# Kernel tuning notes

Hardware: AMD Instinct MI355X
Metric: run time of the kernel (lower is better)

Reference implementation:

```python
import jax, jax.numpy as jnp
import numpy as np

N = 100000
E = 1600000
F_IN = 64
H = 128
D_OUT = 1
G = 512  # number of graphs
EPS = 1e-5


def setup_inputs() -> dict:
    key = jax.random.key(0)
    ks = jax.random.split(key, 16)
    x = jax.random.normal(ks[0], (N, F_IN), dtype=jnp.float32)
    edge_index = jax.random.randint(ks[1], (2, E), 0, N, dtype=jnp.int64)
    batch = jnp.sort(jax.random.randint(ks[2], (N,), 0, G, dtype=jnp.int64))
    def lin(k, fin, fout):
        s = 1.0 / np.sqrt(fin)
        k1, k2 = jax.random.split(k)
        return (jax.random.uniform(k1, (fin, fout), jnp.float32, -s, s),
                jax.random.uniform(k2, (fout,), jnp.float32, -s, s))
    fc1_w, fc1_b = lin(ks[3], F_IN, H)
    gc1_w, gc1_b = lin(ks[4], H, H)
    gc2_w, gc2_b = lin(ks[5], H, H)
    fc2_w, fc2_b = lin(ks[6], H, D_OUT)
    gn1_g = jnp.ones((H,), jnp.float32); gn1_b = jnp.zeros((H,), jnp.float32)
    gn2_g = jnp.ones((H,), jnp.float32); gn2_b = jnp.zeros((H,), jnp.float32)
    return dict(x=x, edge_index=edge_index, batch=batch,
                fc1_w=fc1_w, fc1_b=fc1_b, gc1_w=gc1_w, gc1_b=gc1_b,
                gn1_g=gn1_g, gn1_b=gn1_b, gc2_w=gc2_w, gc2_b=gc2_b,
                gn2_g=gn2_g, gn2_b=gn2_b, fc2_w=fc2_w, fc2_b=fc2_b)


def gcn_conv(x, src, dst, deg_inv_sqrt, w, b):
    # x: [N,H]; symmetric-normalized aggregation with self-loops already in src/dst
    h = x @ w  # [N, H_out]
    norm = deg_inv_sqrt[src] * deg_inv_sqrt[dst]  # [E+N]
    msgs = h[src] * norm[:, None]
    out = jax.ops.segment_sum(msgs, dst, num_segments=N)
    return out + b


def graph_layernorm(x, batch, gamma, beta, counts):
    # PyG LayerNorm mode='graph': normalize over all nodes+channels per graph
    denom = jnp.maximum(counts * x.shape[1], 1.0)  # [G]
    mean = jax.ops.segment_sum(x.sum(-1), batch, num_segments=G) / denom
    xc = x - mean[batch][:, None]
    var = jax.ops.segment_sum((xc * xc).sum(-1), batch, num_segments=G) / denom
    inv = jax.lax.rsqrt(var + EPS)
    return xc * inv[batch][:, None] * gamma + beta


def reference(x, edge_index, batch, fc1_w, fc1_b, gc1_w, gc1_b, gn1_g, gn1_b,
              gc2_w, gc2_b, gn2_g, gn2_b, fc2_w, fc2_b):
    loops = jnp.arange(N, dtype=edge_index.dtype)
    src = jnp.concatenate([edge_index[0], loops])
    dst = jnp.concatenate([edge_index[1], loops])
    deg = jax.ops.segment_sum(jnp.ones_like(dst, dtype=x.dtype), dst, num_segments=N)
    deg_inv_sqrt = jnp.where(deg > 0, jax.lax.rsqrt(jnp.maximum(deg, 1.0)), 0.0)
    counts = jax.ops.segment_sum(jnp.ones_like(batch, dtype=x.dtype), batch, num_segments=G)

    hx = x @ fc1_w + fc1_b
    h = jax.nn.relu(graph_layernorm(gcn_conv(hx, src, dst, deg_inv_sqrt, gc1_w, gc1_b), batch, gn1_g, gn1_b, counts))
    h = jax.nn.relu(graph_layernorm(gcn_conv(h, src, dst, deg_inv_sqrt, gc2_w, gc2_b), batch, gn2_g, gn2_b, counts))
    pooled = jax.ops.segment_sum(h, batch, num_segments=G) / jnp.maximum(counts, 1.0)[:, None]
    return pooled @ fc2_w + fc2_b  # [G, D_OUT]
```

## Files before the change

kernel.cpp:

```cpp
#include <hip/hip_runtime.h>

#define NN 100000
#define EE 1600000
#define FIN 64
#define HH 128
#define GG 512
#define EPSV 1e-5f

__device__ __forceinline__ unsigned short f2bf(float f) {
  unsigned int u = __float_as_uint(f);
  u = (u + 0x7FFFu + ((u >> 16) & 1u)) >> 16;
  return (unsigned short)u;
}

__global__ void initk(int* deg, int* cursor, int* counts,
                      float* gsum1, float* gsq1, float* gsum2, float* gsq2,
                      float* pooled) {
  int i = blockIdx.x * 256 + threadIdx.x;
  if (i < NN) { deg[i] = 1; cursor[i] = 0; }
  if (i < GG) { counts[i] = 0; gsum1[i] = 0.f; gsq1[i] = 0.f; gsum2[i] = 0.f; gsq2[i] = 0.f; }
  if (i < GG * HH) pooled[i] = 0.f;
}

__global__ void convx(const float* __restrict__ x, unsigned short* __restrict__ xb) {
  int i = blockIdx.x * 256 + threadIdx.x;
  if (i >= NN * FIN / 4) return;
  float4 v = reinterpret_cast<const float4*>(x)[i];
  ushort4 o;
  o.x = f2bf(v.x); o.y = f2bf(v.y); o.z = f2bf(v.z); o.w = f2bf(v.w);
  reinterpret_cast<ushort4*>(xb)[i] = o;
}

__global__ void countk(const int* __restrict__ ei, const int* __restrict__ batch,
                       int* deg, int* counts) {
  int i = blockIdx.x * 256 + threadIdx.x;
  if (i < EE) atomicAdd(&deg[ei[EE + i]], 1);
  if (i < NN) atomicAdd(&counts[batch[i]], 1);
}

__global__ void disk(const int* __restrict__ deg, float* __restrict__ dis) {
  int i = blockIdx.x * 256 + threadIdx.x;
  if (i < NN) dis[i] = rsqrtf((float)deg[i]);
}

#define SCHUNK 1024
__global__ void scan1(const int* __restrict__ deg, int* __restrict__ bsum) {
  __shared__ int red[256];
  int b = blockIdx.x, t = threadIdx.x;
  int base = b * SCHUNK + t * 4;
  int s = 0;
#pragma unroll
  for (int i = 0; i < 4; i++) { int idx = base + i; if (idx < NN) s += deg[idx] - 1; }
  red[t] = s; __syncthreads();
  for (int o = 128; o > 0; o >>= 1) { if (t < o) red[t] += red[t + o]; __syncthreads(); }
  if (t == 0) bsum[b] = red[0];
}

__global__ void scan2(const int* __restrict__ bsum, int* __restrict__ boff,
                      int* __restrict__ rowptr, int nblk) {
  if (threadIdx.x == 0 && blockIdx.x == 0) {
    int run = 0;
    for (int i = 0; i < nblk; i++) { boff[i] = run; run += bsum[i]; }
    rowptr[NN] = run;
  }
}

__global__ void scan3(const int* __restrict__ deg, const int* __restrict__ boff,
                      int* __restrict__ rowptr) {
  __shared__ int sc[2][256];
  int b = blockIdx.x, t = threadIdx.x;
  int base = b * SCHUNK + t * 4;
  int v[4]; int s = 0;
#pragma unroll
  for (int i = 0; i < 4; i++) {
    int idx = base + i;
    v[i] = (idx < NN) ? (deg[idx] - 1) : 0;
    s += v[i];
  }
  int pp = 0;
  sc[0][t] = s; __syncthreads();
  for (int o = 1; o < 256; o <<= 1) {
    int val = sc[pp][t];
    if (t >= o) val += sc[pp][t - o];
    sc[pp ^ 1][t] = val; __syncthreads();
    pp ^= 1;
  }
  int excl = sc[pp][t] - s;
  int p = boff[b] + excl;
#pragma unroll
  for (int i = 0; i < 4; i++) {
    int idx = base + i;
    if (idx < NN) rowptr[idx] = p;
    p += v[i];
  }
}

__global__ void scatterk(const int* __restrict__ ei, int* cursor,
                         const int* __restrict__ rowptr, int* __restrict__ colsrc) {
  int e = blockIdx.x * 256 + threadIdx.x;
  if (e >= EE) return;
  int d = ei[EE + e];
  int pos = rowptr[d] + atomicAdd(&cursor[d], 1);
  colsrc[pos] = ei[e];
}

__global__ void prepw(const float* __restrict__ fc1w, const float* __restrict__ fc1b,
                      const float* __restrict__ gc1w,
                      float* __restrict__ Wp, float* __restrict__ c1) {
  int k = blockIdx.x, t = threadIdx.x;
  if (k < 64) {
    float s = 0.f;
    for (int j = 0; j < 128; j++) s = fmaf(fc1w[k * 128 + j], gc1w[j * 128 + t], s);
    Wp[k * 128 + t] = s;
  } else {
    float s = 0.f;
    for (int j = 0; j < 128; j++) s = fmaf(fc1b[j], gc1w[j * 128 + t], s);
    c1[t] = s;
  }
}

__global__ __launch_bounds__(256, 8)
void aggx(const unsigned short* __restrict__ X, const int* __restrict__ colsrc,
          const int* __restrict__ rowptr, const float* __restrict__ dis,
          float* __restrict__ Y, float* __restrict__ rowsum) {
  int wid = threadIdx.x >> 6;
  int n = blockIdx.x * 4 + wid;
  int lane = threadIdx.x & 63;
  int slot = lane >> 3, q = lane & 7;
  float di = dis[n];
  int rp0 = rowptr[n];
  int m = rowptr[n + 1] - rp0 + 1;
  float acc[8];
#pragma unroll
  for (int k = 0; k < 8; k++) acc[k] = 0.f;
  float wsum = 0.f;
  int p = 0;
  for (; p + 15 < m; p += 16) {
    int s[2]; float w[2]; uint4 h[2];
#pragma unroll
    for (int j = 0; j < 2; j++) {
      int idx = p + 8 * j + slot;
      s[j] = (idx == m - 1) ? n : colsrc[rp0 + idx];
    }
#pragma unroll
    for (int j = 0; j < 2; j++) {
      w[j] = dis[s[j]] * di;
      h[j] = reinterpret_cast<const uint4*>(X + (size_t)s[j] * FIN)[q];
    }
#pragma unroll
    for (int j = 0; j < 2; j++) {
      unsigned int u;
      u = h[j].x; acc[0] = fmaf(__uint_as_float(u << 16), w[j], acc[0]);
                  acc[1] = fmaf(__uint_as_float(u & 0xFFFF0000u), w[j], acc[1]);
      u = h[j].y; acc[2] = fmaf(__uint_as_float(u << 16), w[j], acc[2]);
                  acc[3] = fmaf(__uint_as_float(u & 0xFFFF0000u), w[j], acc[3]);
      u = h[j].z; acc[4] = fmaf(__uint_as_float(u << 16), w[j], acc[4]);
                  acc[5] = fmaf(__uint_as_float(u & 0xFFFF0000u), w[j], acc[5]);
      u = h[j].w; acc[6] = fmaf(__uint_as_float(u << 16), w[j], acc[6]);
                  acc[7] = fmaf(__uint_as_float(u & 0xFFFF0000u), w[j], acc[7]);
      wsum += w[j];
    }
  }
  for (; p < m; p += 8) {
    int idx = p + slot;
    if (idx < m) {
      int sv = (idx == m - 1) ? n : colsrc[rp0 + idx];
      float w = dis[sv] * di;
      uint4 h = reinterpret_cast<const uint4*>(X + (size_t)sv * FIN)[q];
      unsigned int u;
      u = h.x; acc[0] = fmaf(__uint_as_float(u << 16), w, acc[0]);
               acc[1] = fmaf(__uint_as_float(u & 0xFFFF0000u), w, acc[1]);
      u = h.y; acc[2] = fmaf(__uint_as_float(u << 16), w, acc[2]);
               acc[3] = fmaf(__uint_as_float(u & 0xFFFF0000u), w, acc[3]);
      u = h.z; acc[4] = fmaf(__uint_as_float(u << 16), w, acc[4]);
               acc[5] = fmaf(__uint_as_float(u & 0xFFFF0000u), w, acc[5]);
      u = h.w; acc[6] = fmaf(__uint_as_float(u << 16), w, acc[6]);
               acc[7] = fmaf(__uint_as_float(u & 0xFFFF0000u), w, acc[7]);
      wsum += w;
    }
  }
#pragma unroll
  for (int o = 8; o <= 32; o <<= 1) {
#pragma unroll
    for (int k = 0; k < 8; k++) acc[k] += __shfl_xor(acc[k], o);
    wsum += __shfl_xor(wsum, o);
  }
  if (slot == 0) {
    float4 a = make_float4(acc[0], acc[1], acc[2], acc[3]);
    float4 b = make_float4(acc[4], acc[5], acc[6], acc[7]);
    reinterpret_cast<float4*>(&Y[(size_t)n * FIN + q * 8])[0] = a;
    reinterpret_cast<float4*>(&Y[(size_t)n * FIN + q * 8])[1] = b;
  }
  if (lane == 0) rowsum[n] = wsum;
}

__global__ void gemmA(const float* __restrict__ Y, const float* __restrict__ Wp,
                      const float* __restrict__ c1, const float* __restrict__ gc1b,
                      const float* __restrict__ rowsum, const int* __restrict__ batch,
                      float* __restrict__ A, float* __restrict__ gsum, float* __restrict__ gsq) {
  __shared__ float ys[8 * 64];
  __shared__ float l1[8][2], l2[8][2];
  int n0 = blockIdx.x * 8, t = threadIdx.x;
  reinterpret_cast<float4*>(ys)[t] =
      reinterpret_cast<const float4*>(Y + (size_t)n0 * 64)[t];
  __syncthreads();
  float cv = c1[t], bv = gc1b[t];
  float acc[8];
#pragma unroll
  for (int n = 0; n < 8; n++) acc[n] = bv;
#pragma unroll 4
  for (int k = 0; k < 64; k++) {
    float wv = Wp[k * 128 + t];
#pragma unroll
    for (int n = 0; n < 8; n++) acc[n] = fmaf(ys[n * 64 + k], wv, acc[n]);
  }
#pragma unroll
  for (int n = 0; n < 8; n++) {
    acc[n] = fmaf(rowsum[n0 + n], cv, acc[n]);
    A[(size_t)(n0 + n) * 128 + t] = acc[n];
  }
  int wid = t >> 6, lane = t & 63;
#pragma unroll
  for (int n = 0; n < 8; n++) {
    float s1v = acc[n], s2v = acc[n] * acc[n];
    for (int o = 32; o > 0; o >>= 1) {
      s1v += __shfl_down(s1v, o);
      s2v += __shfl_down(s2v, o);
    }
    if (lane == 0) { l1[n][wid] = s1v; l2[n][wid] = s2v; }
  }
  __syncthreads();
  if (t < 8) {
    int b = batch[n0 + t];
    atomicAdd(&gsum[b], l1[t][0] + l1[t][1]);
    atomicAdd(&gsq[b], l2[t][0] + l2[t][1]);
  }
}

__global__ void gemm128(const float* __restrict__ X, const float* __restrict__ W,
                        unsigned short* __restrict__ Yb,
                        const int* __restrict__ batch,
                        const float* __restrict__ mean, const float* __restrict__ inv,
                        const float* __restrict__ gamma, const float* __restrict__ beta) {
  __shared__ float xs[8 * 128];
  int n0 = blockIdx.x * 8, t = threadIdx.x;
  const float* xb = X + (size_t)n0 * 128;
#pragma unroll
  for (int j = 0; j < 8; j++) {
    int node = n0 + j;
    int bb = batch[node];
    float v = xb[j * 128 + t];
    v = (v - mean[bb]) * inv[bb] * gamma[t] + beta[t];
    xs[j * 128 + t] = fmaxf(v, 0.f);
  }
  __syncthreads();
  float acc[8];
#pragma unroll
  for (int n = 0; n < 8; n++) acc[n] = 0.f;
#pragma unroll 4
  for (int k = 0; k < 128; k++) {
    float wv = W[k * 128 + t];
#pragma unroll
    for (int n = 0; n < 8; n++) acc[n] = fmaf(xs[n * 128 + k], wv, acc[n]);
  }
#pragma unroll
  for (int n = 0; n < 8; n++) Yb[(size_t)(n0 + n) * 128 + t] = f2bf(acc[n]);
}

__global__ __launch_bounds__(256, 8)
void aggk(const unsigned short* __restrict__ Hin, const int* __restrict__ colsrc,
          const int* __restrict__ rowptr, const float* __restrict__ dis,
          const float* __restrict__ bias, const int* __restrict__ batch,
          float* __restrict__ Yout, float* __restrict__ gsum, float* __restrict__ gsq) {
  int wid = threadIdx.x >> 6;
  int n = blockIdx.x * 4 + wid;
  int lane = threadIdx.x & 63;
  int slot = lane >> 4, q = lane & 15;
  float di = dis[n];
  int rp0 = rowptr[n];
  int m = rowptr[n + 1] - rp0 + 1;
  float acc[8];
#pragma unroll
  for (int k = 0; k < 8; k++) acc[k] = 0.f;
  int p = 0;
  for (; p + 15 < m; p += 16) {
    int s[4]; float w[4]; uint4 h[4];
#pragma unroll
    for (int j = 0; j < 4; j++) {
      int idx = p + 4 * j + slot;
      s[j] = (idx == m - 1) ? n : colsrc[rp0 + idx];
    }
#pragma unroll
    for (int j = 0; j < 4; j++) {
      w[j] = dis[s[j]] * di;
      h[j] = reinterpret_cast<const uint4*>(Hin + (size_t)s[j] * HH)[q];
    }
#pragma unroll
    for (int j = 0; j < 4; j++) {
      unsigned int u;
      u = h[j].x; acc[0] = fmaf(__uint_as_float(u << 16), w[j], acc[0]);
                  acc[1] = fmaf(__uint_as_float(u & 0xFFFF0000u), w[j], acc[1]);
      u = h[j].y; acc[2] = fmaf(__uint_as_float(u << 16), w[j], acc[2]);
                  acc[3] = fmaf(__uint_as_float(u & 0xFFFF0000u), w[j], acc[3]);
      u = h[j].z; acc[4] = fmaf(__uint_as_float(u << 16), w[j], acc[4]);
                  acc[5] = fmaf(__uint_as_float(u & 0xFFFF0000u), w[j], acc[5]);
      u = h[j].w; acc[6] = fmaf(__uint_as_float(u << 16), w[j], acc[6]);
                  acc[7] = fmaf(__uint_as_float(u & 0xFFFF0000u), w[j], acc[7]);
    }
  }
  for (; p < m; p += 4) {
    int idx = p + slot;
    if (idx < m) {
      int sv = (idx == m - 1) ? n : colsrc[rp0 + idx];
      float w = dis[sv] * di;
      uint4 h = reinterpret_cast<const uint4*>(Hin + (size_t)sv * HH)[q];
      unsigned int u;
      u = h.x; acc[0] = fmaf(__uint_as_float(u << 16), w, acc[0]);
               acc[1] = fmaf(__uint_as_float(u & 0xFFFF0000u), w, acc[1]);
      u = h.y; acc[2] = fmaf(__uint_as_float(u << 16), w, acc[2]);
               acc[3] = fmaf(__uint_as_float(u & 0xFFFF0000u), w, acc[3]);
      u = h.z; acc[4] = fmaf(__uint_as_float(u << 16), w, acc[4]);
               acc[5] = fmaf(__uint_as_float(u & 0xFFFF0000u), w, acc[5]);
      u = h.w; acc[6] = fmaf(__uint_as_float(u << 16), w, acc[6]);
               acc[7] = fmaf(__uint_as_float(u & 0xFFFF0000u), w, acc[7]);
    }
  }
#pragma unroll
  for (int o = 16; o <= 32; o <<= 1) {
#pragma unroll
    for (int k = 0; k < 8; k++) acc[k] += __shfl_xor(acc[k], o);
  }
  float4 b0 = reinterpret_cast<const float4*>(&bias[q * 8])[0];
  float4 b1 = reinterpret_cast<const float4*>(&bias[q * 8])[1];
  acc[0] += b0.x; acc[1] += b0.y; acc[2] += b0.z; acc[3] += b0.w;
  acc[4] += b1.x; acc[5] += b1.y; acc[6] += b1.z; acc[7] += b1.w;
  if (slot == 0) {
    float4 a = make_float4(acc[0], acc[1], acc[2], acc[3]);
    float4 b = make_float4(acc[4], acc[5], acc[6], acc[7]);
    reinterpret_cast<float4*>(&Yout[(size_t)n * HH + q * 8])[0] = a;
    reinterpret_cast<float4*>(&Yout[(size_t)n * HH + q * 8])[1] = b;
  }
  float s1 = acc[0] + acc[1] + acc[2] + acc[3] + acc[4] + acc[5] + acc[6] + acc[7];
  float s2 = acc[0] * acc[0] + acc[1] * acc[1] + acc[2] * acc[2] + acc[3] * acc[3] +
             acc[4] * acc[4] + acc[5] * acc[5] + acc[6] * acc[6] + acc[7] * acc[7];
  for (int o = 8; o > 0; o >>= 1) {
    s1 += __shfl_down(s1, o);
    s2 += __shfl_down(s2, o);
  }
  if (lane == 0) {
    int b = batch[n];
    atomicAdd(&gsum[b], s1);
    atomicAdd(&gsq[b], s2);
  }
}

__global__ void lnfinal(const float* __restrict__ gsum, const float* __restrict__ gsq,
                        const int* __restrict__ counts,
                        float* __restrict__ mean, float* __restrict__ inv) {
  int g = blockIdx.x * 256 + threadIdx.x;
  if (g >= GG) return;
  float denom = fmaxf((float)counts[g] * (float)HH, 1.f);
  float m = gsum[g] / denom;
  float v = gsq[g] / denom - m * m;
  mean[g] = m;
  inv[g] = rsqrtf(fmaxf(v, 0.f) + EPSV);
}

__global__ void poolk(const float* __restrict__ A, const int* __restrict__ batch,
                      const float* __restrict__ mean, const float* __restrict__ inv,
                      const float* __restrict__ gamma, const float* __restrict__ beta,
                      float* __restrict__ pooled) {
  int idx = blockIdx.x * 256 + threadIdx.x;
  if (idx >= NN * HH) return;
  int n = idx >> 7, ch = idx & 127;
  int b = batch[n];
  float v = (A[idx] - mean[b]) * inv[b] * gamma[ch] + beta[ch];
  v = fmaxf(v, 0.f);
  atomicAdd(&pooled[b * 128 + ch], v);
}

__global__ void finalk(const float* __restrict__ pooled, const int* __restrict__ counts,
                       const float* __restrict__ w, const float* __restrict__ b,
                       float* __restrict__ out) {
  int g = blockIdx.x, t = threadIdx.x;
  float cnt = fmaxf((float)counts[g], 1.f);
  float v = pooled[g * 128 + t] / cnt * w[t];
  for (int o = 32; o > 0; o >>= 1) v += __shfl_down(v, o);
  __shared__ float l[2];
  if ((t & 63) == 0) l[t >> 6] = v;
  __syncthreads();
  if (t == 0) out[g] = l[0] + l[1] + b[0];
}

extern "C" void kernel_launch(void* const* d_in, const int* in_sizes, int n_in,
                              void* d_out, int out_size, void* d_ws, size_t ws_size,
                              hipStream_t stream) {
  const float* x = (const float*)d_in[0];
  const int* ei = (const int*)d_in[1];
  const int* batch = (const int*)d_in[2];
  const float* fc1_w = (const float*)d_in[3];
  const float* fc1_b = (const float*)d_in[4];
  const float* gc1_w = (const float*)d_in[5];
  const float* gc1_b = (const float*)d_in[6];
  const float* gn1_g = (const float*)d_in[7];
  const float* gn1_b = (const float*)d_in[8];
  const float* gc2_w = (const float*)d_in[9];
  const float* gc2_b = (const float*)d_in[10];
  const float* gn2_g = (const float*)d_in[11];
  const float* gn2_b = (const float*)d_in[12];
  const float* fc2_w = (const float*)d_in[13];
  const float* fc2_b = (const float*)d_in[14];
  float* out = (float*)d_out;

  char* p = (char*)d_ws;
  auto alloc = [&](size_t bytes) { void* r = (void*)p; p += ((bytes + 255) / 256) * 256; return r; };
  float* A = (float*)alloc((size_t)NN * HH * 4);
  float* B = (float*)alloc((size_t)NN * HH * 4);
  float* Yx = B;
  unsigned short* Bb = (unsigned short*)B;
  unsigned short* xb = (unsigned short*)(A + (size_t)NN * 96);
  int* colsrc = (int*)alloc((size_t)EE * 4);
  int* rowptr = (int*)alloc((size_t)(NN + 1) * 4);
  int* deg = (int*)alloc((size_t)NN * 4);
  int* cursor = (int*)alloc((size_t)NN * 4);
  float* dis = (float*)alloc((size_t)NN * 4);
  float* rowsum = (float*)alloc((size_t)NN * 4);
  int* counts = (int*)alloc((size_t)GG * 4);
  float* gsum1 = (float*)alloc((size_t)GG * 4);
  float* gsq1 = (float*)alloc((size_t)GG * 4);
  float* gsum2 = (float*)alloc((size_t)GG * 4);
  float* gsq2 = (float*)alloc((size_t)GG * 4);
  float* mean1 = (float*)alloc((size_t)GG * 4);
  float* inv1 = (float*)alloc((size_t)GG * 4);
  float* mean2 = (float*)alloc((size_t)GG * 4);
  float* inv2 = (float*)alloc((size_t)GG * 4);
  float* pooled = (float*)alloc((size_t)GG * HH * 4);
  float* Wp = (float*)alloc((size_t)64 * 128 * 4);
  float* c1 = (float*)alloc((size_t)128 * 4);
  int* bsum = (int*)alloc(1024);
  int* boff = (int*)alloc(1024);

  int nblk = (NN + SCHUNK - 1) / SCHUNK;

  initk<<<(NN + 255) / 256, 256, 0, stream>>>(deg, cursor, counts, gsum1, gsq1, gsum2, gsq2, pooled);
  convx<<<(NN * FIN / 4 + 255) / 256, 256, 0, stream>>>(x, xb);
  countk<<<(EE + 255) / 256, 256, 0, stream>>>(ei, batch, deg, counts);
  disk<<<(NN + 255) / 256, 256, 0, stream>>>(deg, dis);
  scan1<<<nblk, 256, 0, stream>>>(deg, bsum);
  scan2<<<1, 64, 0, stream>>>(bsum, boff, rowptr, nblk);
  scan3<<<nblk, 256, 0, stream>>>(deg, boff, rowptr);
  scatterk<<<(EE + 255) / 256, 256, 0, stream>>>(ei, cursor, rowptr, colsrc);
  prepw<<<65, 128, 0, stream>>>(fc1_w, fc1_b, gc1_w, Wp, c1);

  aggx<<<NN / 4, 256, 0, stream>>>(xb, colsrc, rowptr, dis, Yx, rowsum);
  gemmA<<<NN / 8, 128, 0, stream>>>(Yx, Wp, c1, gc1_b, rowsum, batch, A, gsum1, gsq1);
  lnfinal<<<(GG + 255) / 256, 256, 0, stream>>>(gsum1, gsq1, counts, mean1, inv1);
  gemm128<<<NN / 8, 128, 0, stream>>>(A, gc2_w, Bb, batch, mean1, inv1, gn1_g, gn1_b);
  aggk<<<NN / 4, 256, 0, stream>>>(Bb, colsrc, rowptr, dis, gc2_b, batch, A, gsum2, gsq2);
  lnfinal<<<(GG + 255) / 256, 256, 0, stream>>>(gsum2, gsq2, counts, mean2, inv2);
  poolk<<<(NN * HH + 255) / 256, 256, 0, stream>>>(A, batch, mean2, inv2, gn2_g, gn2_b, pooled);
  finalk<<<GG, 128, 0, stream>>>(pooled, counts, fc2_w, fc2_b, out);
}
```

Before: 946.2 us.

## Precompute per-edge source norms, unify gather loops, fuse pooling with final projection

Scatter now also stores dis[src] per CSR slot, so the aggregation kernels read a coalesced weight array instead of doing a dependent random gather of dis. The aggregation loops are merged into one masked loop with deeper unroll (3 and 5 rows in flight), dropping the separate tail loop. The atomic-based pooling and the final projection are replaced by one per-graph kernel that relies on sorted batch (via a scan of the graph counts) and folds the fc2 dot product into the reduction. This adds an extra 6.4MB write in scatter and wasted masked loads on short rows.

```diff
diff --git a/kernel.cpp b/kernel.cpp
--- a/kernel.cpp
+++ b/kernel.cpp
@@ -14,12 +14,10 @@
 }
 
 __global__ void initk(int* deg, int* cursor, int* counts,
-                      float* gsum1, float* gsq1, float* gsum2, float* gsq2,
-                      float* pooled) {
+                      float* gsum1, float* gsq1, float* gsum2, float* gsq2) {
   int i = blockIdx.x * 256 + threadIdx.x;
   if (i < NN) { deg[i] = 1; cursor[i] = 0; }
   if (i < GG) { counts[i] = 0; gsum1[i] = 0.f; gsq1[i] = 0.f; gsum2[i] = 0.f; gsq2[i] = 0.f; }
-  if (i < GG * HH) pooled[i] = 0.f;
 }
 
 __global__ void convx(const float* __restrict__ x, unsigned short* __restrict__ xb) {
@@ -95,13 +93,32 @@
   }
 }
 
+__global__ void gscan(const int* __restrict__ counts, int* __restrict__ gstart) {
+  __shared__ int sc[2][GG];
+  int t = threadIdx.x;
+  int v = counts[t];
+  int pp = 0;
+  sc[0][t] = v; __syncthreads();
+  for (int o = 1; o < GG; o <<= 1) {
+    int val = sc[pp][t];
+    if (t >= o) val += sc[pp][t - o];
+    sc[pp ^ 1][t] = val; __syncthreads();
+    pp ^= 1;
+  }
+  gstart[t + 1] = sc[pp][t];
+  if (t == 0) gstart[0] = 0;
+}
+
 __global__ void scatterk(const int* __restrict__ ei, int* cursor,
-                         const int* __restrict__ rowptr, int* __restrict__ colsrc) {
+                         const int* __restrict__ rowptr, const float* __restrict__ dis,
+                         int* __restrict__ colsrc, float* __restrict__ wdis) {
   int e = blockIdx.x * 256 + threadIdx.x;
   if (e >= EE) return;
   int d = ei[EE + e];
+  int src = ei[e];
   int pos = rowptr[d] + atomicAdd(&cursor[d], 1);
-  colsrc[pos] = ei[e];
+  colsrc[pos] = src;
+  wdis[pos] = dis[src];
 }
 
 __global__ void prepw(const float* __restrict__ fc1w, const float* __restrict__ fc1b,
@@ -121,6 +138,7 @@
 
 __global__ __launch_bounds__(256, 8)
 void aggx(const unsigned short* __restrict__ X, const int* __restrict__ colsrc,
+          const float* __restrict__ wdis,
           const int* __restrict__ rowptr, const float* __restrict__ dis,
           float* __restrict__ Y, float* __restrict__ rowsum) {
   int wid = threadIdx.x >> 6;
@@ -134,21 +152,20 @@
 #pragma unroll
   for (int k = 0; k < 8; k++) acc[k] = 0.f;
   float wsum = 0.f;
-  int p = 0;
-  for (; p + 15 < m; p += 16) {
-    int s[2]; float w[2]; uint4 h[2];
-#pragma unroll
-    for (int j = 0; j < 2; j++) {
+  for (int p = 0; p < m; p += 24) {
+    int s[3]; float w[3]; uint4 h[3];
+#pragma unroll
+    for (int j = 0; j < 3; j++) {
       int idx = p + 8 * j + slot;
-      s[j] = (idx == m - 1) ? n : colsrc[rp0 + idx];
+      s[j] = (idx >= m - 1) ? n : colsrc[rp0 + idx];
+      float wp = (idx == m - 1) ? di : wdis[rp0 + idx];
+      w[j] = (idx < m) ? wp * di : 0.f;
     }
 #pragma unroll
-    for (int j = 0; j < 2; j++) {
-      w[j] = dis[s[j]] * di;
+    for (int j = 0; j < 3; j++)
       h[j] = reinterpret_cast<const uint4*>(X + (size_t)s[j] * FIN)[q];
-    }
-#pragma unroll
-    for (int j = 0; j < 2; j++) {
+#pragma unroll
+    for (int j = 0; j < 3; j++) {
       unsigned int u;
       u = h[j].x; acc[0] = fmaf(__uint_as_float(u << 16), w[j], acc[0]);
                   acc[1] = fmaf(__uint_as_float(u & 0xFFFF0000u), w[j], acc[1]);
@@ -159,24 +176,6 @@
       u = h[j].w; acc[6] = fmaf(__uint_as_float(u << 16), w[j], acc[6]);
                   acc[7] = fmaf(__uint_as_float(u & 0xFFFF0000u), w[j], acc[7]);
       wsum += w[j];
-    }
-  }
-  for (; p < m; p += 8) {
-    int idx = p + slot;
-    if (idx < m) {
-      int sv = (idx == m - 1) ? n : colsrc[rp0 + idx];
-      float w = dis[sv] * di;
-      uint4 h = reinterpret_cast<const uint4*>(X + (size_t)sv * FIN)[q];
-      unsigned int u;
-      u = h.x; acc[0] = fmaf(__uint_as_float(u << 16), w, acc[0]);
-               acc[1] = fmaf(__uint_as_float(u & 0xFFFF0000u), w, acc[1]);
-      u = h.y; acc[2] = fmaf(__uint_as_float(u << 16), w, acc[2]);
-               acc[3] = fmaf(__uint_as_float(u & 0xFFFF0000u), w, acc[3]);
-      u = h.z; acc[4] = fmaf(__uint_as_float(u << 16), w, acc[4]);
-               acc[5] = fmaf(__uint_as_float(u & 0xFFFF0000u), w, acc[5]);
-      u = h.w; acc[6] = fmaf(__uint_as_float(u << 16), w, acc[6]);
-               acc[7] = fmaf(__uint_as_float(u & 0xFFFF0000u), w, acc[7]);
-      wsum += w;
     }
   }
 #pragma unroll
@@ -269,6 +268,7 @@
 
 __global__ __launch_bounds__(256, 8)
 void aggk(const unsigned short* __restrict__ Hin, const int* __restrict__ colsrc,
+          const float* __restrict__ wdis,
           const int* __restrict__ rowptr, const float* __restrict__ dis,
           const float* __restrict__ bias, const int* __restrict__ batch,
           float* __restrict__ Yout, float* __restrict__ gsum, float* __restrict__ gsq) {
@@ -282,21 +282,20 @@
   float acc[8];
 #pragma unroll
   for (int k = 0; k < 8; k++) acc[k] = 0.f;
-  int p = 0;
-  for (; p + 15 < m; p += 16) {
-    int s[4]; float w[4]; uint4 h[4];
-#pragma unroll
-    for (int j = 0; j < 4; j++) {
+  for (int p = 0; p < m; p += 20) {
+    int s[5]; float w[5]; uint4 h[5];
+#pragma unroll
+    for (int j = 0; j < 5; j++) {
       int idx = p + 4 * j + slot;
-      s[j] = (idx == m - 1) ? n : colsrc[rp0 + idx];
+      s[j] = (idx >= m - 1) ? n : colsrc[rp0 + idx];
+      float wp = (idx == m - 1) ? di : wdis[rp0 + idx];
+      w[j] = (idx < m) ? wp * di : 0.f;
     }
 #pragma unroll
-    for (int j = 0; j < 4; j++) {
-      w[j] = dis[s[j]] * di;
+    for (int j = 0; j < 5; j++)
       h[j] = reinterpret_cast<const uint4*>(Hin + (size_t)s[j] * HH)[q];
-    }
-#pragma unroll
-    for (int j = 0; j < 4; j++) {
+#pragma unroll
+    for (int j = 0; j < 5; j++) {
       unsigned int u;
       u = h[j].x; acc[0] = fmaf(__uint_as_float(u << 16), w[j], acc[0]);
                   acc[1] = fmaf(__uint_as_float(u & 0xFFFF0000u), w[j], acc[1]);
@@ -308,23 +307,6 @@
                   acc[7] = fmaf(__uint_as_float(u & 0xFFFF0000u), w[j], acc[7]);
     }
   }
-  for (; p < m; p += 4) {
-    int idx = p + slot;
-    if (idx < m) {
-      int sv = (idx == m - 1) ? n : colsrc[rp0 + idx];
-      float w = dis[sv] * di;
-      uint4 h = reinterpret_cast<const uint4*>(Hin + (size_t)sv * HH)[q];
-      unsigned int u;
-      u = h.x; acc[0] = fmaf(__uint_as_float(u << 16), w, acc[0]);
-               acc[1] = fmaf(__uint_as_float(u & 0xFFFF0000u), w, acc[1]);
-      u = h.y; acc[2] = fmaf(__uint_as_float(u << 16), w, acc[2]);
-               acc[3] = fmaf(__uint_as_float(u & 0xFFFF0000u), w, acc[3]);
-      u = h.z; acc[4] = fmaf(__uint_as_float(u << 16), w, acc[4]);
-               acc[5] = fmaf(__uint_as_float(u & 0xFFFF0000u), w, acc[5]);
-      u = h.w; acc[6] = fmaf(__uint_as_float(u << 16), w, acc[6]);
-               acc[7] = fmaf(__uint_as_float(u & 0xFFFF0000u), w, acc[7]);
-    }
-  }
 #pragma unroll
   for (int o = 16; o <= 32; o <<= 1) {
 #pragma unroll
@@ -366,30 +348,29 @@
   inv[g] = rsqrtf(fmaxf(v, 0.f) + EPSV);
 }
 
-__global__ void poolk(const float* __restrict__ A, const int* __restrict__ batch,
-                      const float* __restrict__ mean, const float* __restrict__ inv,
-                      const float* __restrict__ gamma, const float* __restrict__ beta,
-                      float* __restrict__ pooled) {
-  int idx = blockIdx.x * 256 + threadIdx.x;
-  if (idx >= NN * HH) return;
-  int n = idx >> 7, ch = idx & 127;
-  int b = batch[n];
-  float v = (A[idx] - mean[b]) * inv[b] * gamma[ch] + beta[ch];
-  v = fmaxf(v, 0.f);
-  atomicAdd(&pooled[b * 128 + ch], v);
-}
-
-__global__ void finalk(const float* __restrict__ pooled, const int* __restrict__ counts,
-                       const float* __restrict__ w, const float* __restrict__ b,
-                       float* __restrict__ out) {
+__global__ void poolfin(const float* __restrict__ A, const int* __restrict__ gstart,
+                        const int* __restrict__ counts,
+                        const float* __restrict__ mean, const float* __restrict__ inv,
+                        const float* __restrict__ gamma, const float* __restrict__ beta,
+                        const float* __restrict__ w, const float* __restrict__ fb,
+                        float* __restrict__ out) {
   int g = blockIdx.x, t = threadIdx.x;
-  float cnt = fmaxf((float)counts[g], 1.f);
-  float v = pooled[g * 128 + t] / cnt * w[t];
-  for (int o = 32; o > 0; o >>= 1) v += __shfl_down(v, o);
-  __shared__ float l[2];
-  if ((t & 63) == 0) l[t >> 6] = v;
+  int i0 = gstart[g] * HH, i1 = gstart[g + 1] * HH;
+  float m = mean[g], iv = inv[g];
+  float acc = 0.f;
+  for (int i = i0 + t; i < i1; i += 256) {
+    int ch = i & 127;
+    float v = (A[i] - m) * iv * gamma[ch] + beta[ch];
+    acc += fmaxf(v, 0.f) * w[ch];
+  }
+  for (int o = 32; o > 0; o >>= 1) acc += __shfl_down(acc, o);
+  __shared__ float l[4];
+  if ((t & 63) == 0) l[t >> 6] = acc;
   __syncthreads();
-  if (t == 0) out[g] = l[0] + l[1] + b[0];
+  if (t == 0) {
+    float cnt = fmaxf((float)counts[g], 1.f);
+    out[g] = (l[0] + l[1] + l[2] + l[3]) / cnt + fb[0];
+  }
 }
 
 extern "C" void kernel_launch(void* const* d_in, const int* in_sizes, int n_in,
@@ -415,17 +396,19 @@
   char* p = (char*)d_ws;
   auto alloc = [&](size_t bytes) { void* r = (void*)p; p += ((bytes + 255) / 256) * 256; return r; };
   float* A = (float*)alloc((size_t)NN * HH * 4);
-  float* B = (float*)alloc((size_t)NN * HH * 4);
+  float* B = (float*)alloc((size_t)NN * FIN * 4);
   float* Yx = B;
   unsigned short* Bb = (unsigned short*)B;
   unsigned short* xb = (unsigned short*)(A + (size_t)NN * 96);
   int* colsrc = (int*)alloc((size_t)EE * 4);
+  float* wdis = (float*)alloc((size_t)EE * 4);
   int* rowptr = (int*)alloc((size_t)(NN + 1) * 4);
   int* deg = (int*)alloc((size_t)NN * 4);
   int* cursor = (int*)alloc((size_t)NN * 4);
   float* dis = (float*)alloc((size_t)NN * 4);
   float* rowsum = (float*)alloc((size_t)NN * 4);
   int* counts = (int*)alloc((size_t)GG * 4);
+  int* gstart = (int*)alloc((size_t)(GG + 1) * 4);
   float* gsum1 = (float*)alloc((size_t)GG * 4);
   float* gsq1 = (float*)alloc((size_t)GG * 4);
   float* gsum2 = (float*)alloc((size_t)GG * 4);
@@ -434,7 +417,6 @@
   float* inv1 = (float*)alloc((size_t)GG * 4);
   float* mean2 = (float*)alloc((size_t)GG * 4);
   float* inv2 = (float*)alloc((size_t)GG * 4);
-  float* pooled = (float*)alloc((size_t)GG * HH * 4);
   float* Wp = (float*)alloc((size_t)64 * 128 * 4);
   float* c1 = (float*)alloc((size_t)128 * 4);
   int* bsum = (int*)alloc(1024);
@@ -442,22 +424,22 @@
 
   int nblk = (NN + SCHUNK - 1) / SCHUNK;
 
-  initk<<<(NN + 255) / 256, 256, 0, stream>>>(deg, cursor, counts, gsum1, gsq1, gsum2, gsq2, pooled);
+  initk<<<(NN + 255) / 256, 256, 0, stream>>>(deg, cursor, counts, gsum1, gsq1, gsum2, gsq2);
   convx<<<(NN * FIN / 4 + 255) / 256, 256, 0, stream>>>(x, xb);
   countk<<<(EE + 255) / 256, 256, 0, stream>>>(ei, batch, deg, counts);
   disk<<<(NN + 255) / 256, 256, 0, stream>>>(deg, dis);
   scan1<<<nblk, 256, 0, stream>>>(deg, bsum);
   scan2<<<1, 64, 0, stream>>>(bsum, boff, rowptr, nblk);
   scan3<<<nblk, 256, 0, stream>>>(deg, boff, rowptr);
-  scatterk<<<(EE + 255) / 256, 256, 0, stream>>>(ei, cursor, rowptr, colsrc);
+  gscan<<<1, GG, 0, stream>>>(counts, gstart);
+  scatterk<<<(EE + 255) / 256, 256, 0, stream>>>(ei, cursor, rowptr, dis, colsrc, wdis);
   prepw<<<65, 128, 0, stream>>>(fc1_w, fc1_b, gc1_w, Wp, c1);
 
-  aggx<<<NN / 4, 256, 0, stream>>>(xb, colsrc, rowptr, dis, Yx, rowsum);
+  aggx<<<NN / 4, 256, 0, stream>>>(xb, colsrc, wdis, rowptr, dis, Yx, rowsum);
   gemmA<<<NN / 8, 128, 0, stream>>>(Yx, Wp, c1, gc1_b, rowsum, batch, A, gsum1, gsq1);
   lnfinal<<<(GG + 255) / 256, 256, 0, stream>>>(gsum1, gsq1, counts, mean1, inv1);
   gemm128<<<NN / 8, 128, 0, stream>>>(A, gc2_w, Bb, batch, mean1, inv1, gn1_g, gn1_b);
-  aggk<<<NN / 4, 256, 0, stream>>>(Bb, colsrc, rowptr, dis, gc2_b, batch, A, gsum2, gsq2);
+  aggk<<<NN / 4, 256, 0, stream>>>(Bb, colsrc, wdis, rowptr, dis, gc2_b, batch, A, gsum2, gsq2);
   lnfinal<<<(GG + 255) / 256, 256, 0, stream>>>(gsum2, gsq2, counts, mean2, inv2);
-  poolk<<<(NN * HH + 255) / 256, 256, 0, stream>>>(A, batch, mean2, inv2, gn2_g, gn2_b, pooled);
-  finalk<<<GG, 128, 0, stream>>>(pooled, counts, fc2_w, fc2_b, out);
-}
+  poolfin<<<GG, 256, 0, stream>>>(A, gstart, counts, mean2, inv2, gn2_g, gn2_b, fc2_w, fc2_b, out);
+}
```

After: 979.4 us. 1.04x slower.
